# Kernel optimization log

Measured on AMD Instinct MI355X. Metric: run time of the kernel, lower is better.

Reference implementation:

```python
import jax, jax.numpy as jnp
import numpy as np
import math

D = 1024      # d_model
H = 16        # nhead
HD = D // H   # head_dim
FF = 4096     # dim_feedforward
NE = 4        # encoder layers
ND = 4        # decoder layers
S = 1024      # src len
T = 1024      # tgt len
B = 2         # batch
EPS = 1e-5


def _ln(x, g, b):
    m = jnp.mean(x, axis=-1, keepdims=True)
    v = jnp.mean((x - m) ** 2, axis=-1, keepdims=True)
    return (x - m) / jnp.sqrt(v + EPS) * g + b


def _mha(xq, xkv, Wq, Wk, Wv, Wo, bo):
    # xq: [T, B, D], xkv: [S, B, D]
    Tl, Bb, _ = xq.shape
    Sl = xkv.shape[0]
    q = (xq @ Wq.T).reshape(Tl, Bb * H, HD).transpose(1, 0, 2) / math.sqrt(HD)
    k = (xkv @ Wk.T).reshape(Sl, Bb * H, HD).transpose(1, 0, 2)
    v = (xkv @ Wv.T).reshape(Sl, Bb * H, HD).transpose(1, 0, 2)
    attn = jax.nn.softmax(jnp.einsum('zte,zse->zts', q, k), axis=-1)  # [B*H, T, S]
    o = jnp.einsum('zts,zse->zte', attn, v)                            # [B*H, T, HD]
    o = o.transpose(1, 0, 2).reshape(Tl, Bb, D)
    return o @ Wo.T + bo


def _ffn(x, W1, b1, W2, b2):
    return jax.nn.relu(x @ W1.T + b1) @ W2.T + b2


def _forward(src, tgt,
             enc_Wq, enc_Wk, enc_Wv, enc_Wo, enc_bo,
             enc_ln1_g, enc_ln1_b, enc_W1, enc_b1, enc_W2, enc_b2,
             enc_ln2_g, enc_ln2_b, enc_fn_g, enc_fn_b,
             dec_sWq, dec_sWk, dec_sWv, dec_sWo, dec_sbo,
             dec_ln1_g, dec_ln1_b,
             dec_cWq, dec_cWk, dec_cWv, dec_cWo, dec_cbo,
             dec_ln2_g, dec_ln2_b,
             dec_W1, dec_b1, dec_W2, dec_b2,
             dec_ln3_g, dec_ln3_b, dec_fn_g, dec_fn_b):
    # Encoder (post-norm)
    x = src
    for i in range(NE):
        x = _ln(x + _mha(x, x, enc_Wq[i], enc_Wk[i], enc_Wv[i], enc_Wo[i], enc_bo[i]),
                enc_ln1_g[i], enc_ln1_b[i])
        x = _ln(x + _ffn(x, enc_W1[i], enc_b1[i], enc_W2[i], enc_b2[i]),
                enc_ln2_g[i], enc_ln2_b[i])
    memory = _ln(x, enc_fn_g, enc_fn_b)
    # Decoder (post-norm): self-attn, cross-attn, FFN
    y = tgt
    for i in range(ND):
        y = _ln(y + _mha(y, y, dec_sWq[i], dec_sWk[i], dec_sWv[i], dec_sWo[i], dec_sbo[i]),
                dec_ln1_g[i], dec_ln1_b[i])
        y = _ln(y + _mha(y, memory, dec_cWq[i], dec_cWk[i], dec_cWv[i], dec_cWo[i], dec_cbo[i]),
                dec_ln2_g[i], dec_ln2_b[i])
        y = _ln(y + _ffn(y, dec_W1[i], dec_b1[i], dec_W2[i], dec_b2[i]),
                dec_ln3_g[i], dec_ln3_b[i])
    return _ln(y, dec_fn_g, dec_fn_b)


def setup_inputs() -> dict:
    key = jax.random.key(0)
    ks = iter(jax.random.split(key, 128))

    def w(shape, scale=0.02):
        return jax.random.normal(next(ks), shape, dtype=jnp.float32) * scale

    inp = {}
    inp['src'] = jax.random.normal(next(ks), (S, B, D), dtype=jnp.float32)
    inp['tgt'] = jax.random.normal(next(ks), (T, B, D), dtype=jnp.float32)
    # encoder
    inp['enc_Wq'] = w((NE, D, D)); inp['enc_Wk'] = w((NE, D, D)); inp['enc_Wv'] = w((NE, D, D))
    inp['enc_Wo'] = w((NE, D, D)); inp['enc_bo'] = jnp.zeros((NE, D), jnp.float32)
    inp['enc_ln1_g'] = jnp.ones((NE, D), jnp.float32); inp['enc_ln1_b'] = jnp.zeros((NE, D), jnp.float32)
    inp['enc_W1'] = w((NE, FF, D)); inp['enc_b1'] = jnp.zeros((NE, FF), jnp.float32)
    inp['enc_W2'] = w((NE, D, FF)); inp['enc_b2'] = jnp.zeros((NE, D), jnp.float32)
    inp['enc_ln2_g'] = jnp.ones((NE, D), jnp.float32); inp['enc_ln2_b'] = jnp.zeros((NE, D), jnp.float32)
    inp['enc_fn_g'] = jnp.ones((D,), jnp.float32); inp['enc_fn_b'] = jnp.zeros((D,), jnp.float32)
    # decoder
    inp['dec_sWq'] = w((ND, D, D)); inp['dec_sWk'] = w((ND, D, D)); inp['dec_sWv'] = w((ND, D, D))
    inp['dec_sWo'] = w((ND, D, D)); inp['dec_sbo'] = jnp.zeros((ND, D), jnp.float32)
    inp['dec_ln1_g'] = jnp.ones((ND, D), jnp.float32); inp['dec_ln1_b'] = jnp.zeros((ND, D), jnp.float32)
    inp['dec_cWq'] = w((ND, D, D)); inp['dec_cWk'] = w((ND, D, D)); inp['dec_cWv'] = w((ND, D, D))
    inp['dec_cWo'] = w((ND, D, D)); inp['dec_cbo'] = jnp.zeros((ND, D), jnp.float32)
    inp['dec_ln2_g'] = jnp.ones((ND, D), jnp.float32); inp['dec_ln2_b'] = jnp.zeros((ND, D), jnp.float32)
    inp['dec_W1'] = w((ND, FF, D)); inp['dec_b1'] = jnp.zeros((ND, FF), jnp.float32)
    inp['dec_W2'] = w((ND, D, FF)); inp['dec_b2'] = jnp.zeros((ND, D), jnp.float32)
    inp['dec_ln3_g'] = jnp.ones((ND, D), jnp.float32); inp['dec_ln3_b'] = jnp.zeros((ND, D), jnp.float32)
    inp['dec_fn_g'] = jnp.ones((D,), jnp.float32); inp['dec_fn_b'] = jnp.zeros((D,), jnp.float32)
    return inp


def reference(src, tgt,
              enc_Wq, enc_Wk, enc_Wv, enc_Wo, enc_bo,
              enc_ln1_g, enc_ln1_b, enc_W1, enc_b1, enc_W2, enc_b2,
              enc_ln2_g, enc_ln2_b, enc_fn_g, enc_fn_b,
              dec_sWq, dec_sWk, dec_sWv, dec_sWo, dec_sbo,
              dec_ln1_g, dec_ln1_b,
              dec_cWq, dec_cWk, dec_cWv, dec_cWo, dec_cbo,
              dec_ln2_g, dec_ln2_b,
              dec_W1, dec_b1, dec_W2, dec_b2,
              dec_ln3_g, dec_ln3_b, dec_fn_g, dec_fn_b):
    return _forward(src, tgt,
                    enc_Wq, enc_Wk, enc_Wv, enc_Wo, enc_bo,
                    enc_ln1_g, enc_ln1_b, enc_W1, enc_b1, enc_W2, enc_b2,
                    enc_ln2_g, enc_ln2_b, enc_fn_g, enc_fn_b,
                    dec_sWq, dec_sWk, dec_sWv, dec_sWo, dec_sbo,
                    dec_ln1_g, dec_ln1_b,
                    dec_cWq, dec_cWk, dec_cWv, dec_cWo, dec_cbo,
                    dec_ln2_g, dec_ln2_b,
                    dec_W1, dec_b1, dec_W2, dec_b2,
                    dec_ln3_g, dec_ln3_b, dec_fn_g, dec_fn_b)
```

## Files before the change

kernel.cpp:

```cpp
#include <hip/hip_runtime.h>

#define DI __device__ __forceinline__

typedef __attribute__((ext_vector_type(4))) float f32x4;
typedef __attribute__((ext_vector_type(8))) short short8;
typedef __attribute__((ext_vector_type(4))) short s16x4;
typedef unsigned short u16;
typedef unsigned long long u64;

#define GLDS(gp, lp)                                              \
  __builtin_amdgcn_global_load_lds(                               \
      (const __attribute__((address_space(1))) void*)(gp),        \
      (__attribute__((address_space(3))) void*)(lp), 16, 0, 0)

DI u16 f2bf(float f) {
  unsigned u = __builtin_bit_cast(unsigned, f);
  u += 0x7fffu + ((u >> 16) & 1u);
  return (u16)(u >> 16);
}
DI float bf2f(u16 h) {
  unsigned u = ((unsigned)h) << 16;
  return __builtin_bit_cast(float, u);
}

template <int MODE>
__global__ __launch_bounds__(256, 2) void gemm_bt(
    const u16* __restrict__ Ap, const u16* __restrict__ Ap2,
    const u16* __restrict__ Bp, void* __restrict__ Cp, void* __restrict__ Cp2,
    void* __restrict__ Cp3, const float* __restrict__ bias, int N, int lda,
    int ldb, int kz, int NT, long sB, long sC, float scale) {
  constexpr int BM = 128, BN = 128;
  constexpr int WM = BM / 2, WN = BN / 2, FM = WM / 16, FN = WN / 16;
  constexpr int ATILE = BM * 128, TILE = ATILE + BN * 128;

  __shared__ char smem[2 * TILE];

  const int tid = threadIdx.x;
  const int wid = tid >> 6, lane = tid & 63;
  const int z = blockIdx.z;
  const long bm = (long)blockIdx.y * BM;
  const long bn = (long)blockIdx.x * BN;
  const int kofs = z * kz;

  const u16* A16 = (MODE == 2 && z > 0) ? Ap2 : Ap;
  const u16* B16 = Bp + (long)z * sB;

  const int lrow = lane >> 3;
  const int lslot = (lane & 7) ^ lrow;
  const u16* asrc0 = A16 + (bm + lrow) * (long)lda + kofs + lslot * 8;
  const u16* bsrc0 = B16 + (bn + lrow) * (long)ldb + kofs + lslot * 8;

  auto stage = [&](int kt, char* buf) {
    const u16* as = asrc0 + kt * 64;
    const u16* bs = bsrc0 + kt * 64;
#pragma unroll
    for (int c = 0; c < 4; c++) {
      int chunk = wid * 4 + c;
      GLDS(as + (long)chunk * 8 * lda, buf + chunk * 1024);
    }
#pragma unroll
    for (int c = 0; c < 4; c++) {
      int chunk = wid * 4 + c;
      GLDS(bs + (long)chunk * 8 * ldb, buf + ATILE + chunk * 1024);
    }
  };

  const int wm = wid >> 1, wn = wid & 1;
  const int l15 = lane & 15, ks = lane >> 4;

  f32x4 acc[FM][FN];
#pragma unroll
  for (int i = 0; i < FM; i++)
#pragma unroll
    for (int j = 0; j < FN; j++) acc[i][j] = (f32x4){0.f, 0.f, 0.f, 0.f};

  auto compute = [&](const char* buf) {
    const char* As = buf;
    const char* Bs = buf + ATILE;
#pragma unroll
    for (int kk = 0; kk < 2; kk++) {
      short8 af[FM], bfr[FN];
#pragma unroll
      for (int i = 0; i < FM; i++) {
        int row = wm * WM + i * 16 + l15;
        int byte = row * 128 + kk * 64 + ks * 16;
        byte ^= (row & 7) << 4;
        af[i] = *(const short8*)(As + byte);
      }
#pragma unroll
      for (int j = 0; j < FN; j++) {
        int row = wn * WN + j * 16 + l15;
        int byte = row * 128 + kk * 64 + ks * 16;
        byte ^= (row & 7) << 4;
        bfr[j] = *(const short8*)(Bs + byte);
      }
#pragma unroll
      for (int i = 0; i < FM; i++)
#pragma unroll
        for (int j = 0; j < FN; j++)
          acc[i][j] = __builtin_amdgcn_mfma_f32_16x16x32_bf16(af[i], bfr[j],
                                                              acc[i][j], 0, 0, 0);
    }
  };

  stage(0, smem);
  __syncthreads();
  for (int t = 0; t < NT; ++t) {
    char* cur = smem + (t & 1) * TILE;
    char* nxt = smem + ((t + 1) & 1) * TILE;
    if (t + 1 < NT) stage(t + 1, nxt);
    compute(cur);
    __syncthreads();
  }

  if constexpr (MODE == 2) {
    if (z == 2) {
      char* tb = smem;
#pragma unroll
      for (int i = 0; i < FM; i++) {
#pragma unroll
        for (int j = 0; j < FN; j++) {
          int np = wn * 64 + j * 16 + l15;
          int basem = wm * 64 + i * 16 + ks * 4;
          unsigned lo = (unsigned)f2bf(acc[i][j][0]) |
                        ((unsigned)f2bf(acc[i][j][2]) << 16);
          unsigned hi = (unsigned)f2bf(acc[i][j][1]) |
                        ((unsigned)f2bf(acc[i][j][3]) << 16);
          int byte0 = np * 256 + basem;
          int byte1 = np * 256 + 128 + basem;
          byte0 ^= (np & 7) << 4;
          byte1 ^= (np & 7) << 4;
          *(unsigned*)(tb + byte0) = lo;
          *(unsigned*)(tb + byte1) = hi;
        }
      }
      __syncthreads();
      const int np = tid >> 1, bsel = tid & 1;
      const int h_ = (int)((bn + np) >> 6), d_ = (int)((bn + np) & 63);
      u16* dst = (u16*)Cp3 + ((long)(bsel * 16 + h_) * 64 + d_) * 1024 +
                 (bm >> 1);
#pragma unroll
      for (int c = 0; c < 8; c++) {
        int byte = np * 256 + bsel * 128 + c * 16;
        byte ^= (np & 7) << 4;
        *(short8*)(dst + c * 8) = *(const short8*)(tb + byte);
      }
      return;
    }
  }

  const float scl = (MODE == 2 && z > 0) ? 1.f : scale;
#pragma unroll
  for (int i = 0; i < FM; i++) {
#pragma unroll
    for (int j = 0; j < FN; j++) {
#pragma unroll
      for (int r = 0; r < 4; r++) {
        long m = bm + wm * WM + i * 16 + ks * 4 + r;
        long n = bn + wn * WN + j * 16 + l15;
        float val = acc[i][j][r] * scl;
        if constexpr (MODE == 0) {
          ((float*)Cp)[z * sC + m * (long)N + n] = val;
        } else if constexpr (MODE == 1) {
          val += bias[n];
          ((u16*)Cp)[m * (long)N + n] = f2bf(fmaxf(val, 0.f));
        } else if constexpr (MODE == 2) {
          u16* Cz = (u16*)(z == 0 ? Cp : Cp2);
          long t_ = m >> 1;
          int b_ = (int)(m & 1), h_ = (int)(n >> 6), d_ = (int)(n & 63);
          Cz[(((long)(b_ * 16 + h_) * 1024 + t_) << 6) + d_] = f2bf(val);
        }
      }
    }
  }
}

__global__ __launch_bounds__(256) void castw_k(const float* __restrict__ a,
                                               const float* __restrict__ b,
                                               const float* __restrict__ c,
                                               const float* __restrict__ d,
                                               u16* __restrict__ out,
                                               long per) {
  const int y = blockIdx.y;
  const float* s = y == 0 ? a : (y == 1 ? b : (y == 2 ? c : d));
  const long i = ((long)blockIdx.x * 256 + threadIdx.x) * 4;
  f32x4 v = *(const f32x4*)(s + i);
  s16x4 hh;
#pragma unroll
  for (int j = 0; j < 4; j++) hh[j] = (short)f2bf(v[j]);
  *(s16x4*)(out + y * per + i) = hh;
}

__global__ __launch_bounds__(256, 2) void flash_k(
    const u16* __restrict__ q, const u16* __restrict__ kb,
    const u16* __restrict__ vt, u16* __restrict__ ab) {
  __shared__ char Ks[2][8192];
  __shared__ char Vs[2][8192];
  __shared__ char P_lds[4][2048];
  __shared__ float stats[4][16];

  const int tid = threadIdx.x;
  const int wid = tid >> 6, lane = tid & 63;
  const int l15 = lane & 15, ks = lane >> 4;
  const int z = blockIdx.y;
  const int q0 = blockIdx.x * 64 + wid * 16;

  const u16* Qz = q + (long)z * 65536;
  const u16* Kz = kb + (long)z * 65536;
  const u16* Vz = vt + (long)z * 65536;
  char* Pw = P_lds[wid];
  float* st = stats[wid];

  const int r_l = lane >> 3;
  const int swsl = ((lane & 7) ^ r_l) * 8;

  auto stageKV = [&](int t, int buf) {
    const int kv0 = t * 64;
#pragma unroll
    for (int c = 0; c < 2; c++) {
      int chunk = wid * 2 + c;
      GLDS(Kz + (long)(kv0 + chunk * 8 + r_l) * 64 + swsl,
           Ks[buf] + chunk * 1024);
      GLDS(Vz + (long)(chunk * 8 + r_l) * 1024 + kv0 + swsl,
           Vs[buf] + chunk * 1024);
    }
  };

  short8 qf[2];
#pragma unroll
  for (int kk = 0; kk < 2; kk++)
    qf[kk] = *(const short8*)(Qz + (q0 + l15) * 64 + kk * 32 + ks * 8);

  f32x4 Oacc[4];
#pragma unroll
  for (int nf = 0; nf < 4; nf++) Oacc[nf] = (f32x4){0.f, 0.f, 0.f, 0.f};
  float mrun = -1e30f, lrun = 0.f;

  stageKV(0, 0);
  __syncthreads();
  for (int t = 0; t < 16; ++t) {
    const int cur = t & 1;
    if (t + 1 < 16) stageKV(t + 1, cur ^ 1);
    f32x4 s[4];
#pragma unroll
    for (int m = 0; m < 4; m++) s[m] = (f32x4){0.f, 0.f, 0.f, 0.f};
#pragma unroll
    for (int kk = 0; kk < 2; kk++) {
#pragma unroll
      for (int m = 0; m < 4; m++) {
        int row = m * 16 + l15;
        int byte = row * 128 + kk * 64 + ks * 16;
        byte ^= (row & 7) << 4;
        short8 kf = *(const short8*)(Ks[cur] + byte);
        s[m] = __builtin_amdgcn_mfma_f32_16x16x32_bf16(kf, qf[kk], s[m], 0, 0, 0);
      }
    }
    float tmax = s[0][0];
#pragma unroll
    for (int m = 0; m < 4; m++)
#pragma unroll
      for (int r = 0; r < 4; r++) tmax = fmaxf(tmax, s[m][r]);
    tmax = fmaxf(tmax, __shfl_xor(tmax, 16));
    tmax = fmaxf(tmax, __shfl_xor(tmax, 32));
    const float mnew = fmaxf(mrun, tmax);
    const float factor = __expf(mrun - mnew);
    float psum = 0.f;
#pragma unroll
    for (int m = 0; m < 4; m++) {
      u16 p4[4];
#pragma unroll
      for (int r = 0; r < 4; r++) {
        float e = __expf(s[m][r] - mnew);
        psum += e;
        p4[r] = f2bf(e);
      }
      u64 pk = (u64)p4[0] | ((u64)p4[1] << 16) | ((u64)p4[2] << 32) |
               ((u64)p4[3] << 48);
      int byte = l15 * 128 + m * 32 + ks * 8;
      byte ^= (l15 & 7) << 4;
      *(u64*)(Pw + byte) = pk;
    }
    psum += __shfl_xor(psum, 16);
    psum += __shfl_xor(psum, 32);
    lrun = lrun * factor + psum;
    mrun = mnew;
    if (ks == 0) st[l15] = factor;
    f32x4 facv = *(const f32x4*)&st[ks * 4];
#pragma unroll
    for (int nf = 0; nf < 4; nf++)
#pragma unroll
      for (int r = 0; r < 4; r++) Oacc[nf][r] *= facv[r];
#pragma unroll
    for (int kk = 0; kk < 2; kk++) {
      int pb = l15 * 128 + kk * 64 + ks * 16;
      pb ^= (l15 & 7) << 4;
      short8 pa = *(const short8*)(Pw + pb);
#pragma unroll
      for (int nf = 0; nf < 4; nf++) {
        int row = nf * 16 + l15;
        int vb_ = row * 128 + kk * 64 + ks * 16;
        vb_ ^= (row & 7) << 4;
        short8 vf = *(const short8*)(Vs[cur] + vb_);
        Oacc[nf] = __builtin_amdgcn_mfma_f32_16x16x32_bf16(pa, vf, Oacc[nf],
                                                           0, 0, 0);
      }
    }
    __syncthreads();
  }
  if (ks == 0) st[l15] = 1.f / lrun;
  f32x4 invv = *(const f32x4*)&st[ks * 4];
  const int b_ = z >> 4, h_ = z & 15;
#pragma unroll
  for (int nf = 0; nf < 4; nf++) {
#pragma unroll
    for (int r = 0; r < 4; r++) {
      int qg = q0 + ks * 4 + r;
      ab[((long)(qg * 2 + b_) << 10) + h_ * 64 + nf * 16 + l15] =
          f2bf(Oacc[nf][r] * invv[r]);
    }
  }
}

template <int NP>
__global__ __launch_bounds__(256) void add_ln_k(
    const u16* __restrict__ x, const float* __restrict__ parts,
    const float* __restrict__ cb, const float* __restrict__ g,
    const float* __restrict__ b, u16* __restrict__ outh,
    float* __restrict__ outf) {
  const long row = blockIdx.x;
  const int tid = threadIdx.x;
  const long base = row * 1024 + tid * 4;
  s16x4 xh = *(const s16x4*)(x + base);
  f32x4 v;
#pragma unroll
  for (int j = 0; j < 4; j++) v[j] = bf2f((u16)xh[j]);
#pragma unroll
  for (int p = 0; p < NP; p++) {
    f32x4 q = *(const f32x4*)(parts + (long)p * 2048 * 1024 + base);
    v[0] += q[0]; v[1] += q[1]; v[2] += q[2]; v[3] += q[3];
  }
  if (cb) {
    f32x4 q = *(const f32x4*)(cb + tid * 4);
    v[0] += q[0]; v[1] += q[1]; v[2] += q[2]; v[3] += q[3];
  }
  float s = v[0] + v[1] + v[2] + v[3];
  float s2 = v[0] * v[0] + v[1] * v[1] + v[2] * v[2] + v[3] * v[3];
#pragma unroll
  for (int off = 1; off < 64; off <<= 1) {
    s += __shfl_xor(s, off);
    s2 += __shfl_xor(s2, off);
  }
  __shared__ float ps[8];
  const int wid = tid >> 6, lane = tid & 63;
  if (lane == 0) {
    ps[wid] = s;
    ps[4 + wid] = s2;
  }
  __syncthreads();
  s = ps[0] + ps[1] + ps[2] + ps[3];
  s2 = ps[4] + ps[5] + ps[6] + ps[7];
  float mean = s * (1.f / 1024.f);
  float var = s2 * (1.f / 1024.f) - mean * mean;
  float rstd = rsqrtf(var + 1e-5f);
  f32x4 gg = *(const f32x4*)(g + tid * 4);
  f32x4 bb = *(const f32x4*)(b + tid * 4);
  f32x4 o;
#pragma unroll
  for (int j = 0; j < 4; j++) o[j] = (v[j] - mean) * rstd * gg[j] + bb[j];
  s16x4 hh;
#pragma unroll
  for (int j = 0; j < 4; j++) hh[j] = (short)f2bf(o[j]);
  *(s16x4*)(outh + base) = hh;
  if (outf) *(f32x4*)(outf + base) = o;
}

__global__ __launch_bounds__(256) void cast_k(const float* __restrict__ in,
                                              u16* __restrict__ o16) {
  const long i = ((long)blockIdx.x * 256 + threadIdx.x) * 4;
  f32x4 v = *(const f32x4*)(in + i);
  s16x4 hh;
#pragma unroll
  for (int j = 0; j < 4; j++) hh[j] = (short)f2bf(v[j]);
  *(s16x4*)(o16 + i) = hh;
}

extern "C" void kernel_launch(void* const* d_in, const int* in_sizes, int n_in,
                              void* d_out, int out_size, void* d_ws,
                              size_t ws_size, hipStream_t stream) {
  const float* src = (const float*)d_in[0];
  const float* tgt = (const float*)d_in[1];
  const float* enc_Wq = (const float*)d_in[2];
  const float* enc_Wk = (const float*)d_in[3];
  const float* enc_Wv = (const float*)d_in[4];
  const float* enc_Wo = (const float*)d_in[5];
  const float* enc_bo = (const float*)d_in[6];
  const float* enc_ln1_g = (const float*)d_in[7];
  const float* enc_ln1_b = (const float*)d_in[8];
  const float* enc_W1 = (const float*)d_in[9];
  const float* enc_b1 = (const float*)d_in[10];
  const float* enc_W2 = (const float*)d_in[11];
  const float* enc_b2 = (const float*)d_in[12];
  const float* enc_ln2_g = (const float*)d_in[13];
  const float* enc_ln2_b = (const float*)d_in[14];
  const float* enc_fn_g = (const float*)d_in[15];
  const float* enc_fn_b = (const float*)d_in[16];
  const float* dec_sWq = (const float*)d_in[17];
  const float* dec_sWk = (const float*)d_in[18];
  const float* dec_sWv = (const float*)d_in[19];
  const float* dec_sWo = (const float*)d_in[20];
  const float* dec_sbo = (const float*)d_in[21];
  const float* dec_ln1_g = (const float*)d_in[22];
  const float* dec_ln1_b = (const float*)d_in[23];
  const float* dec_cWq = (const float*)d_in[24];
  const float* dec_cWk = (const float*)d_in[25];
  const float* dec_cWv = (const float*)d_in[26];
  const float* dec_cWo = (const float*)d_in[27];
  const float* dec_cbo = (const float*)d_in[28];
  const float* dec_ln2_g = (const float*)d_in[29];
  const float* dec_ln2_b = (const float*)d_in[30];
  const float* dec_W1 = (const float*)d_in[31];
  const float* dec_b1 = (const float*)d_in[32];
  const float* dec_W2 = (const float*)d_in[33];
  const float* dec_b2 = (const float*)d_in[34];
  const float* dec_ln3_g = (const float*)d_in[35];
  const float* dec_ln3_b = (const float*)d_in[36];
  const float* dec_fn_g = (const float*)d_in[37];
  const float* dec_fn_b = (const float*)d_in[38];

  char* ws = (char*)d_ws;
  size_t off = 0;
  auto alloc = [&](size_t bytes) {
    void* p = ws + off;
    off += (bytes + 255) & ~(size_t)255;
    return p;
  };
  u16* xh = (u16*)alloc(2048L * 1024 * 2);
  u16* memh = (u16*)alloc(2048L * 1024 * 2);
  u16* h = (u16*)alloc(2048L * 4096 * 2);
  u16* q = (u16*)alloc(2048L * 1024 * 2);
  u16* kb = (u16*)alloc(2048L * 1024 * 2);
  u16* vt = (u16*)alloc(2048L * 1024 * 2);
  u16* ab = (u16*)alloc(2048L * 1024 * 2);
  float* parts = (float*)alloc(4L * 2048 * 1024 * 4);
  u16* wbuf = (u16*)alloc(8L * 1024 * 1024 * 2);
  u16* wbig = (u16*)alloc(112L * 1024 * 1024 * 2);
  const bool mega = off <= ws_size;

  const long sP = 2048L * 1024;
  const long M1 = 1024L * 1024, M4 = 4L * 1024 * 1024;
  u16* encA = wbig;
  u16* encF = wbig + 16 * M1;
  u16* decS = wbig + 48 * M1;
  u16* decC = wbig + 64 * M1;
  u16* decF = wbig + 80 * M1;

  if (mega) {
    castw_k<<<dim3(4096, 4), 256, 0, stream>>>(enc_Wq, enc_Wk, enc_Wv, enc_Wo,
                                               encA, 4 * M1);
    castw_k<<<dim3(16384, 2), 256, 0, stream>>>(enc_W1, enc_W2, enc_W1, enc_W1,
                                                encF, 16 * M1);
    castw_k<<<dim3(4096, 4), 256, 0, stream>>>(dec_sWq, dec_sWk, dec_sWv,
                                               dec_sWo, decS, 4 * M1);
    castw_k<<<dim3(4096, 4), 256, 0, stream>>>(dec_cWq, dec_cWk, dec_cWv,
                                               dec_cWo, decC, 4 * M1);
    castw_k<<<dim3(16384, 2), 256, 0, stream>>>(dec_W1, dec_W2, dec_W1, dec_W1,
                                                decF, 16 * M1);
  }

  auto attn = [&](const u16* qin, const u16* kvin, const float* Wq,
                  const float* Wk, const float* Wv, const float* Wo,
                  const u16* bqkv, long sBq, const u16* bo) {
    if (!mega) {
      castw_k<<<dim3(1024, 4), 256, 0, stream>>>(Wq, Wk, Wv, Wo, wbuf, M1);
      bqkv = wbuf; sBq = M1; bo = wbuf + 3 * M1;
    }
    gemm_bt<2><<<dim3(8, 16, 3), 256, 0, stream>>>(
        qin, kvin, bqkv, q, kb, vt, nullptr,
        1024, 1024, 1024, 0, 16, sBq, 0, 0.125f);
    flash_k<<<dim3(16, 32), 256, 0, stream>>>(q, kb, vt, ab);
    gemm_bt<0><<<dim3(8, 16, 4), 256, 0, stream>>>(
        ab, nullptr, bo, parts, nullptr, nullptr, nullptr,
        1024, 1024, 1024, 256, 4, 0, sP, 1.f);
  };
  auto ffn = [&](const u16* xin, const float* W1, const float* b1,
                 const float* W2, const u16* bw1, const u16* bw2) {
    if (!mega) {
      castw_k<<<dim3(4096, 2), 256, 0, stream>>>(W1, W2, W1, W1, wbuf, M4);
      bw1 = wbuf; bw2 = wbuf + M4;
    }
    gemm_bt<1><<<dim3(32, 16, 1), 256, 0, stream>>>(
        xin, nullptr, bw1, h, nullptr, nullptr, b1,
        4096, 1024, 1024, 0, 16, 0, 0, 1.f);
    gemm_bt<0><<<dim3(8, 16, 4), 256, 0, stream>>>(
        h, nullptr, bw2, parts, nullptr, nullptr, nullptr,
        1024, 4096, 4096, 1024, 16, 0, sP, 1.f);
  };

  const long DD = 1024L * 1024, Dv = 1024, FFD = 4096L * 1024, FFv = 4096;

  cast_k<<<dim3(2048), 256, 0, stream>>>(src, xh);
  for (int i = 0; i < 4; i++) {
    attn(xh, xh, enc_Wq + i * DD, enc_Wk + i * DD, enc_Wv + i * DD,
         enc_Wo + i * DD, encA + i * M1, 4 * M1, encA + 12 * M1 + i * M1);
    add_ln_k<4><<<dim3(2048), 256, 0, stream>>>(
        xh, parts, enc_bo + i * Dv, enc_ln1_g + i * Dv, enc_ln1_b + i * Dv,
        xh, nullptr);
    ffn(xh, enc_W1 + i * FFD, enc_b1 + i * FFv, enc_W2 + i * FFD,
        encF + i * M4, encF + 16 * M1 + i * M4);
    add_ln_k<4><<<dim3(2048), 256, 0, stream>>>(
        xh, parts, enc_b2 + i * Dv, enc_ln2_g + i * Dv, enc_ln2_b + i * Dv,
        xh, nullptr);
  }
  add_ln_k<0><<<dim3(2048), 256, 0, stream>>>(
      xh, nullptr, nullptr, enc_fn_g, enc_fn_b, memh, nullptr);

  cast_k<<<dim3(2048), 256, 0, stream>>>(tgt, xh);
  for (int i = 0; i < 4; i++) {
    attn(xh, xh, dec_sWq + i * DD, dec_sWk + i * DD, dec_sWv + i * DD,
         dec_sWo + i * DD, decS + i * M1, 4 * M1, decS + 12 * M1 + i * M1);
    add_ln_k<4><<<dim3(2048), 256, 0, stream>>>(
        xh, parts, dec_sbo + i * Dv, dec_ln1_g + i * Dv, dec_ln1_b + i * Dv,
        xh, nullptr);
    attn(xh, memh, dec_cWq + i * DD, dec_cWk + i * DD, dec_cWv + i * DD,
         dec_cWo + i * DD, decC + i * M1, 4 * M1, decC + 12 * M1 + i * M1);
    add_ln_k<4><<<dim3(2048), 256, 0, stream>>>(
        xh, parts, dec_cbo + i * Dv, dec_ln2_g + i * Dv, dec_ln2_b + i * Dv,
        xh, nullptr);
    ffn(xh, dec_W1 + i * FFD, dec_b1 + i * FFv, dec_W2 + i * FFD,
        decF + i * M4, decF + 16 * M1 + i * M4);
    add_ln_k<4><<<dim3(2048), 256, 0, stream>>>(
        xh, parts, dec_b2 + i * Dv, dec_ln3_g + i * Dv, dec_ln3_b + i * Dv,
        xh, nullptr);
  }
  add_ln_k<0><<<dim3(2048), 256, 0, stream>>>(
      xh, nullptr, nullptr, dec_fn_g, dec_fn_b, xh, (float*)d_out);
}
```

Baseline: 1.440 ms.

## Single-buffer GEMM LDS for higher occupancy, add XCD swizzle, fuse weight casts

The GEMM drops from a double-buffered LDS tile to a single buffer and raises launch bounds to four blocks per CU. Latency is meant to be hidden by more resident workgroups instead of in-block prefetch, at the cost of an extra barrier per k-step. GEMM and flash-attention blocks are remapped so consecutive tiles land on the same XCD, for L2 locality. The five weight-cast launches are merged into one kernel that selects its source segment from a pointer table.

Result: slower. 1.526 ms (+5.9%).

```diff
diff --git a/kernel.cpp b/kernel.cpp
--- a/kernel.cpp
+++ b/kernel.cpp
@@ -23,8 +23,21 @@
   return __builtin_bit_cast(float, u);
 }
 
+DI void xcd_swz(int& bx, int& by, int& bz) {
+  const int nx = gridDim.x, ny = gridDim.y, nz = gridDim.z;
+  const int nwg = nx * ny * nz;
+  if (nwg & 7) { bx = blockIdx.x; by = blockIdx.y; bz = blockIdx.z; return; }
+  int lin = blockIdx.x + nx * (blockIdx.y + ny * blockIdx.z);
+  const int cpx = nwg >> 3;
+  int s = (lin & 7) * cpx + (lin >> 3);
+  bx = s % nx;
+  int r = s / nx;
+  by = r % ny;
+  bz = r / ny;
+}
+
 template <int MODE>
-__global__ __launch_bounds__(256, 2) void gemm_bt(
+__global__ __launch_bounds__(256, 4) void gemm_bt(
     const u16* __restrict__ Ap, const u16* __restrict__ Ap2,
     const u16* __restrict__ Bp, void* __restrict__ Cp, void* __restrict__ Cp2,
     void* __restrict__ Cp3, const float* __restrict__ bias, int N, int lda,
@@ -33,13 +46,15 @@
   constexpr int WM = BM / 2, WN = BN / 2, FM = WM / 16, FN = WN / 16;
   constexpr int ATILE = BM * 128, TILE = ATILE + BN * 128;
 
-  __shared__ char smem[2 * TILE];
-
+  __shared__ char smem[TILE];
+
+  int bx, by, bz;
+  xcd_swz(bx, by, bz);
   const int tid = threadIdx.x;
   const int wid = tid >> 6, lane = tid & 63;
-  const int z = blockIdx.z;
-  const long bm = (long)blockIdx.y * BM;
-  const long bn = (long)blockIdx.x * BN;
+  const int z = bz;
+  const long bm = (long)by * BM;
+  const long bn = (long)bx * BN;
   const int kofs = z * kz;
 
   const u16* A16 = (MODE == 2 && z > 0) ? Ap2 : Ap;
@@ -50,18 +65,18 @@
   const u16* asrc0 = A16 + (bm + lrow) * (long)lda + kofs + lslot * 8;
   const u16* bsrc0 = B16 + (bn + lrow) * (long)ldb + kofs + lslot * 8;
 
-  auto stage = [&](int kt, char* buf) {
+  auto stage = [&](int kt) {
     const u16* as = asrc0 + kt * 64;
     const u16* bs = bsrc0 + kt * 64;
 #pragma unroll
     for (int c = 0; c < 4; c++) {
       int chunk = wid * 4 + c;
-      GLDS(as + (long)chunk * 8 * lda, buf + chunk * 1024);
+      GLDS(as + (long)chunk * 8 * lda, smem + chunk * 1024);
     }
 #pragma unroll
     for (int c = 0; c < 4; c++) {
       int chunk = wid * 4 + c;
-      GLDS(bs + (long)chunk * 8 * ldb, buf + ATILE + chunk * 1024);
+      GLDS(bs + (long)chunk * 8 * ldb, smem + ATILE + chunk * 1024);
     }
   };
 
@@ -74,9 +89,9 @@
 #pragma unroll
     for (int j = 0; j < FN; j++) acc[i][j] = (f32x4){0.f, 0.f, 0.f, 0.f};
 
-  auto compute = [&](const char* buf) {
-    const char* As = buf;
-    const char* Bs = buf + ATILE;
+  auto compute = [&]() {
+    const char* As = smem;
+    const char* Bs = smem + ATILE;
 #pragma unroll
     for (int kk = 0; kk < 2; kk++) {
       short8 af[FM], bfr[FN];
@@ -103,14 +118,12 @@
     }
   };
 
-  stage(0, smem);
-  __syncthreads();
+  stage(0);
   for (int t = 0; t < NT; ++t) {
-    char* cur = smem + (t & 1) * TILE;
-    char* nxt = smem + ((t + 1) & 1) * TILE;
-    if (t + 1 < NT) stage(t + 1, nxt);
-    compute(cur);
     __syncthreads();
+    compute();
+    __syncthreads();
+    if (t + 1 < NT) stage(t + 1);
   }
 
   if constexpr (MODE == 2) {
@@ -175,6 +188,25 @@
   }
 }
 
+struct WPtrs { const float* p[16]; };
+
+__global__ __launch_bounds__(256) void castw_all(WPtrs w,
+                                                 u16* __restrict__ out) {
+  const int cumM[17] = {0, 4, 8, 12, 16, 32, 48, 52, 56, 60,
+                        64, 68, 72, 76, 80, 96, 112};
+  const long elem = ((long)blockIdx.x * 256 + threadIdx.x) * 4;
+  const int em = (int)(elem >> 20);
+  int seg = 0;
+#pragma unroll
+  for (int i = 1; i < 17; i++) seg += (em >= cumM[i]) ? 1 : 0;
+  const float* s = w.p[seg] + (elem - ((long)cumM[seg] << 20));
+  f32x4 v = *(const f32x4*)s;
+  s16x4 hh;
+#pragma unroll
+  for (int j = 0; j < 4; j++) hh[j] = (short)f2bf(v[j]);
+  *(s16x4*)(out + elem) = hh;
+}
+
 __global__ __launch_bounds__(256) void castw_k(const float* __restrict__ a,
                                                const float* __restrict__ b,
                                                const float* __restrict__ c,
@@ -199,11 +231,13 @@
   __shared__ char P_lds[4][2048];
   __shared__ float stats[4][16];
 
+  int bx, by, bz;
+  xcd_swz(bx, by, bz);
   const int tid = threadIdx.x;
   const int wid = tid >> 6, lane = tid & 63;
   const int l15 = lane & 15, ks = lane >> 4;
-  const int z = blockIdx.y;
-  const int q0 = blockIdx.x * 64 + wid * 16;
+  const int z = by;
+  const int q0 = bx * 64 + wid * 16;
 
   const u16* Qz = q + (long)z * 65536;
   const u16* Kz = kb + (long)z * 65536;
@@ -455,16 +489,13 @@
   u16* decF = wbig + 80 * M1;
 
   if (mega) {
-    castw_k<<<dim3(4096, 4), 256, 0, stream>>>(enc_Wq, enc_Wk, enc_Wv, enc_Wo,
-                                               encA, 4 * M1);
-    castw_k<<<dim3(16384, 2), 256, 0, stream>>>(enc_W1, enc_W2, enc_W1, enc_W1,
-                                                encF, 16 * M1);
-    castw_k<<<dim3(4096, 4), 256, 0, stream>>>(dec_sWq, dec_sWk, dec_sWv,
-                                               dec_sWo, decS, 4 * M1);
-    castw_k<<<dim3(4096, 4), 256, 0, stream>>>(dec_cWq, dec_cWk, dec_cWv,
-                                               dec_cWo, decC, 4 * M1);
-    castw_k<<<dim3(16384, 2), 256, 0, stream>>>(dec_W1, dec_W2, dec_W1, dec_W1,
-                                                decF, 16 * M1);
+    WPtrs wp;
+    wp.p[0] = enc_Wq;  wp.p[1] = enc_Wk;  wp.p[2] = enc_Wv;  wp.p[3] = enc_Wo;
+    wp.p[4] = enc_W1;  wp.p[5] = enc_W2;
+    wp.p[6] = dec_sWq; wp.p[7] = dec_sWk; wp.p[8] = dec_sWv; wp.p[9] = dec_sWo;
+    wp.p[10] = dec_cWq; wp.p[11] = dec_cWk; wp.p[12] = dec_cWv;
+    wp.p[13] = dec_cWo; wp.p[14] = dec_W1; wp.p[15] = dec_W2;
+    castw_all<<<dim3(114688), 256, 0, stream>>>(wp, wbig);
   }
 
   auto attn = [&](const u16* qin, const u16* kvin, const float* Wq,
```
